# Optimization experiments

Hardware: AMD Instinct MI355X
Metric: run time of the kernel (lower is better)

## Reference

```python
import jax, jax.numpy as jnp
import numpy as np

LATENT = 128   # latent_size
FDIM = 32      # feature_dim per plane
FSIZE = 512    # feature_size -> grid is (FSIZE+1)^2
HID = 256      # hidden_dim
N = 500000     # number of query points
IN_DIM = 3
G = FSIZE + 1
SDF_IN = 3 * FDIM + LATENT + IN_DIM  # 227


def setup_inputs() -> dict:
    key = jax.random.key(0)
    ks = jax.random.split(key, 6)
    x = jax.random.normal(ks[0], (N, LATENT + IN_DIM), jnp.float32)
    # 3 tri-planes, each [FDIM, G, G], init randn*0.01 as in FeaturePlanes
    P = jax.random.normal(ks[1], (3, FDIM, G, G), jnp.float32) * 0.01

    def lin(k, fan_in, fan_out):
        s = 1.0 / np.sqrt(fan_in)
        kw, kb = jax.random.split(k)
        W = jax.random.uniform(kw, (fan_in, fan_out), jnp.float32, -s, s)
        b = jax.random.uniform(kb, (fan_out,), jnp.float32, -s, s)
        return W, b

    W0, b0 = lin(ks[2], SDF_IN, HID)
    W1, b1 = lin(ks[3], HID, HID)
    W2, b2 = lin(ks[4], HID, 1)
    return dict(x=x, P=P, W0=W0, b0=b0, W1=W1, b1=b1, W2=W2, b2=b2)


def _sample_plane(plane, uv):
    """Bilinear grid_sample, align_corners=True, padding_mode='border'.
    plane: [C, G, G]; uv: [Npts, 2] with uv[:,0]->width(x), uv[:,1]->height(y).
    Returns [Npts, C]."""
    g = jnp.clip((uv + 1.0) * 0.5 * (G - 1), 0.0, G - 1)  # unnormalize + border clamp
    gx, gy = g[:, 0], g[:, 1]
    x0f, y0f = jnp.floor(gx), jnp.floor(gy)
    x0 = x0f.astype(jnp.int32)
    y0 = y0f.astype(jnp.int32)
    x1 = jnp.minimum(x0 + 1, G - 1)
    y1 = jnp.minimum(y0 + 1, G - 1)
    wx = gx - x0f
    wy = gy - y0f
    v00 = plane[:, y0, x0]  # [C, Npts]
    v01 = plane[:, y0, x1]
    v10 = plane[:, y1, x0]
    v11 = plane[:, y1, x1]
    top = v00 * (1.0 - wx) + v01 * wx
    bot = v10 * (1.0 - wx) + v11 * wx
    return (top * (1.0 - wy) + bot * wy).T  # [Npts, C]


def reference(x, P, W0, b0, W1, b1, W2, b2):
    in_latents = x[:, :LATENT]
    in_x = x[:, -3:]
    coords = jax.lax.stop_gradient(in_x)  # matches .detach() before grid_sample
    # dimension pairs (0,1), (0,2), (1,2) -> one bilinear lookup each, vmapped
    uv = jnp.stack([coords[:, [0, 1]], coords[:, [0, 2]], coords[:, [1, 2]]])  # [3,N,2]
    feats = jax.vmap(_sample_plane)(P, uv)              # [3, N, FDIM]
    feats = jnp.transpose(feats, (1, 0, 2)).reshape(x.shape[0], 3 * FDIM)
    net_in = jnp.concatenate([in_latents, in_x, feats], axis=-1)  # [N, 227]
    h = jax.nn.relu(net_in @ W0 + b0)
    h = jax.nn.relu(h @ W1 + b1)
    out = (h @ W2 + b2).squeeze(-1)  # [N]
    return out
```

## Files before the change

kernel.cpp:

```cpp
#include <hip/hip_runtime.h>
#include <stdint.h>

#define XDIM 131
#define LATENT 128
#define FDIM 32
#define GSZ 513
#define SDF_IN 227
#define FEAT0 136
#define TROWS 64
#define BSTRIDE 1040

typedef __attribute__((ext_vector_type(8))) short bf16x8;
typedef __attribute__((ext_vector_type(4))) float f32x4;
typedef unsigned int uint32;

__device__ __forceinline__ unsigned short f2bf(float f) {
  uint32 u = __float_as_uint(f);
  u += 0x7fffu + ((u >> 16) & 1u);
  return (unsigned short)(u >> 16);
}
__device__ __forceinline__ float bf2f(unsigned short s) {
  return __uint_as_float(((uint32)s) << 16);
}
__device__ __forceinline__ uint32 pk2bf(float a, float b) {
  return (uint32)f2bf(a) | ((uint32)f2bf(b) << 16);
}

__device__ __forceinline__ int slot16(int r) { return (r * 16) ^ (((r >> 3) & 1) << 5); }
__device__ __forceinline__ int blk_of(int c) { return (c >> 5) * 4 + ((c >> 3) & 3); }
__device__ __forceinline__ int act_byte(int r, int c) {
  return blk_of(c) * BSTRIDE + slot16(r) + (c & 7) * 2;
}

__global__ void prep_pt(const float* __restrict__ P, unsigned short* __restrict__ Pt) {
  int i = blockIdx.x * 256 + threadIdx.x;
  const int CELLS = 3 * GSZ * GSZ;
  if (i >= CELLS) return;
  int pl = i / (GSZ * GSZ);
  int yx = i - pl * (GSZ * GSZ);
  const float* src = P + (size_t)pl * FDIM * GSZ * GSZ + yx;
  const size_t GG = (size_t)GSZ * GSZ;
  uint4* dst = (uint4*)(Pt + (size_t)i * 32);
#pragma unroll
  for (int w = 0; w < 4; ++w) {
    uint4 t;
    t.x = pk2bf(src[(w * 8 + 0) * GG], src[(w * 8 + 1) * GG]);
    t.y = pk2bf(src[(w * 8 + 2) * GG], src[(w * 8 + 3) * GG]);
    t.z = pk2bf(src[(w * 8 + 4) * GG], src[(w * 8 + 5) * GG]);
    t.w = pk2bf(src[(w * 8 + 6) * GG], src[(w * 8 + 7) * GG]);
    dst[w] = t;
  }
}

__global__ void prep_w(const float* __restrict__ W0, const float* __restrict__ W1,
                       unsigned short* __restrict__ W0g, unsigned short* __restrict__ W1g) {
  int i = blockIdx.x * 256 + threadIdx.x;
  int sel = i >> 13;
  int t = i & 8191;
  int kb = t >> 10;
  int g  = (t >> 8) & 3;
  int n  = t & 255;
  float vv[8];
#pragma unroll
  for (int j = 0; j < 8; ++j) {
    int k = kb * 32 + g * 8 + j;
    float val;
    if (sel == 0) {
      int src = (k < 131) ? k : ((k >= FEAT0 && k < FEAT0 + 96) ? k - 5 : -1);
      val = (src >= 0) ? W0[src * 256 + n] : 0.f;
    } else {
      val = W1[k * 256 + n];
    }
    vv[j] = val;
  }
  uint4 o;
  o.x = pk2bf(vv[0], vv[1]);
  o.y = pk2bf(vv[2], vv[3]);
  o.z = pk2bf(vv[4], vv[5]);
  o.w = pk2bf(vv[6], vv[7]);
  unsigned short* dst = (sel == 0 ? W0g : W1g) + (size_t)t * 8;
  *(uint4*)dst = o;
}

__device__ __forceinline__ void gemm_layer(unsigned char* actb,
                                           const unsigned short* __restrict__ Wg,
                                           const float* __restrict__ bias,
                                           int cg, int lr, int lg)
{
  f32x4 acc[4][4];
#pragma unroll
  for (int mf = 0; mf < 4; ++mf)
#pragma unroll
    for (int nf = 0; nf < 4; ++nf) acc[mf][nf] = (f32x4){0.f, 0.f, 0.f, 0.f};

  float bs[4];
#pragma unroll
  for (int nf = 0; nf < 4; ++nf) bs[nf] = bias[cg * 64 + nf * 16 + lr];

#pragma unroll
  for (int kb = 0; kb < 8; ++kb) {
    bf16x8 a[4];
    const int ab = (kb * 4 + lg) * BSTRIDE;
#pragma unroll
    for (int mf = 0; mf < 4; ++mf)
      a[mf] = *(const bf16x8*)(actb + ab + slot16(mf * 16 + lr));
    const unsigned short* wb = Wg + (size_t)(kb * 4 + lg) * 2048 + (size_t)(cg * 64 + lr) * 8;
#pragma unroll
    for (int nf = 0; nf < 4; ++nf) {
      bf16x8 b = *(const bf16x8*)(wb + nf * 128);
#pragma unroll
      for (int mf = 0; mf < 4; ++mf)
        acc[mf][nf] = __builtin_amdgcn_mfma_f32_16x16x32_bf16(a[mf], b, acc[mf][nf], 0, 0, 0);
    }
  }
  __syncthreads();
#pragma unroll
  for (int mf = 0; mf < 4; ++mf)
#pragma unroll
    for (int nf = 0; nf < 4; ++nf) {
      int c = cg * 64 + nf * 16 + lr;
      unsigned char* dst = actb + blk_of(c) * BSTRIDE + (c & 7) * 2;
#pragma unroll
      for (int reg = 0; reg < 4; ++reg) {
        int r = mf * 16 + lg * 4 + reg;
        float vv = fmaxf(acc[mf][nf][reg] + bs[nf], 0.f);
        *(unsigned short*)(dst + slot16(r)) = f2bf(vv);
      }
    }
  __syncthreads();
}

template<int USE_PT>
__global__ __launch_bounds__(256, 4) void sdf_main(
    const float* __restrict__ x, const float* __restrict__ P,
    const unsigned short* __restrict__ Pt,
    const unsigned short* __restrict__ W0g, const unsigned short* __restrict__ W1g,
    const float* __restrict__ b0, const float* __restrict__ b1,
    const float* __restrict__ W2, const float* __restrict__ b2v,
    float* __restrict__ out, int Npts)
{
  __shared__ __align__(16) unsigned char actb[32 * BSTRIDE];

  const int tid = threadIdx.x;
  const int p0 = blockIdx.x * TROWS;

  for (int z = tid; z < 260; z += 256) {
    uint4 zz = {0u, 0u, 0u, 0u};
    if (z < 65) ((uint4*)(actb + 16 * BSTRIDE))[z] = zz;
    else        ((uint4*)(actb + 29 * BSTRIDE))[z - 65] = zz;
  }
  __syncthreads();

#pragma unroll 1
  for (int i = 0; i < 4; ++i) {
    int t = i * 256 + tid;
    int cb = t & 15, r = t >> 4;
    int p = min(p0 + r, Npts - 1);
    const float* src = x + (size_t)p * XDIM + cb * 8;
    uint4 v;
    v.x = pk2bf(src[0], src[1]);
    v.y = pk2bf(src[2], src[3]);
    v.z = pk2bf(src[4], src[5]);
    v.w = pk2bf(src[6], src[7]);
    *(uint4*)(actb + cb * BSTRIDE + slot16(r)) = v;
  }
  if (tid < TROWS) {
    int r = tid;
    int p = min(p0 + r, Npts - 1);
#pragma unroll
    for (int j = 0; j < 3; ++j)
      *(unsigned short*)(actb + act_byte(r, 128 + j)) = f2bf(x[(size_t)p * XDIM + 128 + j]);
  }

  {
    int p_l = tid >> 2;
    int q = tid & 3;
    int p = min(p0 + p_l, Npts - 1);
    const float* xr = x + (size_t)p * XDIM + LATENT;
    float cc0 = xr[0], cc1 = xr[1], cc2 = xr[2];
#pragma unroll
    for (int pl = 0; pl < 3; ++pl) {
      float u = (pl == 2) ? cc1 : cc0;
      float v = (pl == 0) ? cc1 : cc2;
      float gx = fminf(fmaxf((u + 1.f) * 256.f, 0.f), 512.f);
      float gy = fminf(fmaxf((v + 1.f) * 256.f, 0.f), 512.f);
      float x0f = floorf(gx), y0f = floorf(gy);
      int x0 = (int)x0f, y0 = (int)y0f;
      int x1 = min(x0 + 1, GSZ - 1), y1 = min(y0 + 1, GSZ - 1);
      float wx = gx - x0f, wy = gy - y0f;
      float w00 = (1.f - wx) * (1.f - wy), w01 = wx * (1.f - wy);
      float w10 = (1.f - wx) * wy,        w11 = wx * wy;
      const unsigned short* pb = Pt + (size_t)pl * GSZ * GSZ * 32 + q * 8;
      bf16x8 v00 = *(const bf16x8*)(pb + (size_t)(y0 * GSZ + x0) * 32);
      bf16x8 v01 = *(const bf16x8*)(pb + (size_t)(y0 * GSZ + x1) * 32);
      bf16x8 v10 = *(const bf16x8*)(pb + (size_t)(y1 * GSZ + x0) * 32);
      bf16x8 v11 = *(const bf16x8*)(pb + (size_t)(y1 * GSZ + x1) * 32);
      float f[8];
#pragma unroll
      for (int j = 0; j < 8; ++j) {
        f[j] = w00 * bf2f((unsigned short)v00[j])
             + w01 * bf2f((unsigned short)v01[j])
             + w10 * bf2f((unsigned short)v10[j])
             + w11 * bf2f((unsigned short)v11[j]);
      }
      uint4 fv;
      fv.x = pk2bf(f[0], f[1]);
      fv.y = pk2bf(f[2], f[3]);
      fv.z = pk2bf(f[4], f[5]);
      fv.w = pk2bf(f[6], f[7]);
      *(uint4*)(actb + (17 + pl * 4 + q) * BSTRIDE + slot16(p_l)) = fv;
    }
  }
  __syncthreads();

  const int lane = tid & 63, wid = tid >> 6;
  const int lr = lane & 15, lg = lane >> 4;

  gemm_layer(actb, W0g, b0, wid, lr, lg);
  gemm_layer(actb, W1g, b1, wid, lr, lg);

  {
    int p_l = tid >> 2, q = tid & 3;
    float sum = 0.f;
#pragma unroll 2
    for (int m = 0; m < 8; ++m) {
      int cbase = m * 32 + q * 8;
      bf16x8 h = *(const bf16x8*)(actb + (m * 4 + q) * BSTRIDE + slot16(p_l));
      float4 wa = *(const float4*)(W2 + cbase);
      float4 wb = *(const float4*)(W2 + cbase + 4);
      sum += bf2f((unsigned short)h[0]) * wa.x + bf2f((unsigned short)h[1]) * wa.y
           + bf2f((unsigned short)h[2]) * wa.z + bf2f((unsigned short)h[3]) * wa.w
           + bf2f((unsigned short)h[4]) * wb.x + bf2f((unsigned short)h[5]) * wb.y
           + bf2f((unsigned short)h[6]) * wb.z + bf2f((unsigned short)h[7]) * wb.w;
    }
    sum += __shfl_xor(sum, 1);
    sum += __shfl_xor(sum, 2);
    if (q == 0) {
      int p = p0 + p_l;
      if (p < Npts) out[p] = sum + b2v[0];
    }
  }
}

extern "C" void kernel_launch(void* const* d_in, const int* in_sizes, int n_in,
                              void* d_out, int out_size, void* d_ws, size_t ws_size,
                              hipStream_t stream)
{
  const float* x  = (const float*)d_in[0];
  const float* P  = (const float*)d_in[1];
  const float* W0 = (const float*)d_in[2];
  const float* b0 = (const float*)d_in[3];
  const float* W1 = (const float*)d_in[4];
  const float* b1 = (const float*)d_in[5];
  const float* W2 = (const float*)d_in[6];
  const float* b2 = (const float*)d_in[7];
  float* out = (float*)d_out;
  int Npts = in_sizes[0] / XDIM;

  const size_t PT_BYTES = (size_t)3 * GSZ * GSZ * 32 * 2;
  const size_t WG_BYTES = (size_t)8192 * 8 * 2;
  char* ws = (char*)d_ws;
  int use_pt = (ws_size >= PT_BYTES + 2 * WG_BYTES) ? 1 : 0;
  unsigned short *Ptb, *W0g, *W1g;
  if (use_pt) {
    Ptb = (unsigned short*)ws;
    W0g = (unsigned short*)(ws + PT_BYTES);
    W1g = (unsigned short*)(ws + PT_BYTES + WG_BYTES);
  } else {
    Ptb = nullptr;
    W0g = (unsigned short*)ws;
    W1g = (unsigned short*)(ws + WG_BYTES);
  }

  prep_w<<<64, 256, 0, stream>>>(W0, W1, W0g, W1g);
  if (use_pt) prep_pt<<<(3 * GSZ * GSZ + 255) / 256, 256, 0, stream>>>(P, Ptb);

  int nblk = (Npts + TROWS - 1) / TROWS;
  if (use_pt)
    sdf_main<1><<<nblk, 256, 0, stream>>>(x, P, Ptb, W0g, W1g, b0, b1, W2, b2, out, Npts);
  else
    sdf_main<0><<<nblk, 256, 0, stream>>>(x, P, Ptb, W0g, W1g, b0, b1, W2, b2, out, Npts);
}
```

Before: 333.7 us.

## Split tri-plane gather into separate kernel and widen MLP blocks to 512 threads

Adds a standalone gather kernel that computes the bilinear tri-plane features into a bf16 workspace buffer, which the MLP kernel then copies into shared memory. The MLP kernel now runs 512 threads (8 waves), each wave owning 32 output columns instead of 64, to raise latency hiding and occupancy. The aim is to decouple the latency-bound random gathers from the MFMA GEMM phase. It costs an extra global write and read of roughly 96 MB of features plus one more launch, and it depends on the workspace being large enough, with fallback modes kept for smaller workspaces.

Result: no change. 330.0 us (-1.1%).

```diff
diff --git a/kernel.cpp b/kernel.cpp
--- a/kernel.cpp
+++ b/kernel.cpp
@@ -3,14 +3,13 @@
 
 #define XDIM 131
 #define LATENT 128
-#define FDIM 32
 #define GSZ 513
-#define SDF_IN 227
 #define FEAT0 136
 #define TROWS 64
 #define BSTRIDE 1040
 
 typedef __attribute__((ext_vector_type(8))) short bf16x8;
+typedef __attribute__((ext_vector_type(4))) short bf16x4;
 typedef __attribute__((ext_vector_type(4))) float f32x4;
 typedef unsigned int uint32;
 
@@ -28,9 +27,6 @@
 
 __device__ __forceinline__ int slot16(int r) { return (r * 16) ^ (((r >> 3) & 1) << 5); }
 __device__ __forceinline__ int blk_of(int c) { return (c >> 5) * 4 + ((c >> 3) & 3); }
-__device__ __forceinline__ int act_byte(int r, int c) {
-  return blk_of(c) * BSTRIDE + slot16(r) + (c & 7) * 2;
-}
 
 __global__ void prep_pt(const float* __restrict__ P, unsigned short* __restrict__ Pt) {
   int i = blockIdx.x * 256 + threadIdx.x;
@@ -38,7 +34,7 @@
   if (i >= CELLS) return;
   int pl = i / (GSZ * GSZ);
   int yx = i - pl * (GSZ * GSZ);
-  const float* src = P + (size_t)pl * FDIM * GSZ * GSZ + yx;
+  const float* src = P + (size_t)pl * 32 * GSZ * GSZ + yx;
   const size_t GG = (size_t)GSZ * GSZ;
   uint4* dst = (uint4*)(Pt + (size_t)i * 32);
 #pragma unroll
@@ -82,20 +78,75 @@
   *(uint4*)dst = o;
 }
 
+__global__ __launch_bounds__(256) void k_gather(
+    const float* __restrict__ x, const unsigned short* __restrict__ Pt,
+    unsigned short* __restrict__ feats, int Npts)
+{
+  int idx = blockIdx.x * 256 + threadIdx.x;
+  int p = min(idx >> 2, Npts - 1);
+  int q = idx & 3;
+  const float* xr = x + (size_t)p * XDIM + LATENT;
+  float cc0 = xr[0], cc1 = xr[1], cc2 = xr[2];
+
+  const unsigned short* pp[12];
+  float w[12];
+#pragma unroll
+  for (int pl = 0; pl < 3; ++pl) {
+    float u = (pl == 2) ? cc1 : cc0;
+    float v = (pl == 0) ? cc1 : cc2;
+    float gx = fminf(fmaxf((u + 1.f) * 256.f, 0.f), 512.f);
+    float gy = fminf(fmaxf((v + 1.f) * 256.f, 0.f), 512.f);
+    float x0f = floorf(gx), y0f = floorf(gy);
+    int x0 = (int)x0f, y0 = (int)y0f;
+    int x1 = min(x0 + 1, GSZ - 1), y1 = min(y0 + 1, GSZ - 1);
+    float wx = gx - x0f, wy = gy - y0f;
+    w[pl * 4 + 0] = (1.f - wx) * (1.f - wy);
+    w[pl * 4 + 1] = wx * (1.f - wy);
+    w[pl * 4 + 2] = (1.f - wx) * wy;
+    w[pl * 4 + 3] = wx * wy;
+    const unsigned short* pb = Pt + (size_t)pl * GSZ * GSZ * 32 + q * 8;
+    pp[pl * 4 + 0] = pb + (size_t)(y0 * GSZ + x0) * 32;
+    pp[pl * 4 + 1] = pb + (size_t)(y0 * GSZ + x1) * 32;
+    pp[pl * 4 + 2] = pb + (size_t)(y1 * GSZ + x0) * 32;
+    pp[pl * 4 + 3] = pb + (size_t)(y1 * GSZ + x1) * 32;
+  }
+  bf16x8 v[12];
+#pragma unroll
+  for (int j = 0; j < 12; ++j) v[j] = *(const bf16x8*)pp[j];
+
+#pragma unroll
+  for (int pl = 0; pl < 3; ++pl) {
+    float f[8];
+#pragma unroll
+    for (int j = 0; j < 8; ++j) {
+      f[j] = w[pl * 4 + 0] * bf2f((unsigned short)v[pl * 4 + 0][j])
+           + w[pl * 4 + 1] * bf2f((unsigned short)v[pl * 4 + 1][j])
+           + w[pl * 4 + 2] * bf2f((unsigned short)v[pl * 4 + 2][j])
+           + w[pl * 4 + 3] * bf2f((unsigned short)v[pl * 4 + 3][j]);
+    }
+    uint4 fv;
+    fv.x = pk2bf(f[0], f[1]);
+    fv.y = pk2bf(f[2], f[3]);
+    fv.z = pk2bf(f[4], f[5]);
+    fv.w = pk2bf(f[6], f[7]);
+    *(uint4*)(feats + (size_t)p * 96 + pl * 32 + q * 8) = fv;
+  }
+}
+
 __device__ __forceinline__ void gemm_layer(unsigned char* actb,
                                            const unsigned short* __restrict__ Wg,
                                            const float* __restrict__ bias,
                                            int cg, int lr, int lg)
 {
-  f32x4 acc[4][4];
+  f32x4 acc[4][2];
 #pragma unroll
   for (int mf = 0; mf < 4; ++mf)
 #pragma unroll
-    for (int nf = 0; nf < 4; ++nf) acc[mf][nf] = (f32x4){0.f, 0.f, 0.f, 0.f};
-
-  float bs[4];
-#pragma unroll
-  for (int nf = 0; nf < 4; ++nf) bs[nf] = bias[cg * 64 + nf * 16 + lr];
+    for (int nf = 0; nf < 2; ++nf) acc[mf][nf] = (f32x4){0.f, 0.f, 0.f, 0.f};
+
+  float bs[2];
+#pragma unroll
+  for (int nf = 0; nf < 2; ++nf) bs[nf] = bias[cg * 32 + nf * 16 + lr];
 
 #pragma unroll
   for (int kb = 0; kb < 8; ++kb) {
@@ -104,9 +155,9 @@
 #pragma unroll
     for (int mf = 0; mf < 4; ++mf)
       a[mf] = *(const bf16x8*)(actb + ab + slot16(mf * 16 + lr));
-    const unsigned short* wb = Wg + (size_t)(kb * 4 + lg) * 2048 + (size_t)(cg * 64 + lr) * 8;
-#pragma unroll
-    for (int nf = 0; nf < 4; ++nf) {
+    const unsigned short* wb = Wg + (size_t)(kb * 4 + lg) * 2048 + (size_t)(cg * 32 + lr) * 8;
+#pragma unroll
+    for (int nf = 0; nf < 2; ++nf) {
       bf16x8 b = *(const bf16x8*)(wb + nf * 128);
 #pragma unroll
       for (int mf = 0; mf < 4; ++mf)
@@ -117,8 +168,8 @@
 #pragma unroll
   for (int mf = 0; mf < 4; ++mf)
 #pragma unroll
-    for (int nf = 0; nf < 4; ++nf) {
-      int c = cg * 64 + nf * 16 + lr;
+    for (int nf = 0; nf < 2; ++nf) {
+      int c = cg * 32 + nf * 16 + lr;
       unsigned char* dst = actb + blk_of(c) * BSTRIDE + (c & 7) * 2;
 #pragma unroll
       for (int reg = 0; reg < 4; ++reg) {
@@ -130,10 +181,10 @@
   __syncthreads();
 }
 
-template<int USE_PT>
-__global__ __launch_bounds__(256, 4) void sdf_main(
+template<int MODE>
+__global__ __launch_bounds__(512, 4) void sdf_mlp(
     const float* __restrict__ x, const float* __restrict__ P,
-    const unsigned short* __restrict__ Pt,
+    const unsigned short* __restrict__ Pt, const unsigned short* __restrict__ feats,
     const unsigned short* __restrict__ W0g, const unsigned short* __restrict__ W1g,
     const float* __restrict__ b0, const float* __restrict__ b1,
     const float* __restrict__ W2, const float* __restrict__ b2v,
@@ -144,16 +195,16 @@
   const int tid = threadIdx.x;
   const int p0 = blockIdx.x * TROWS;
 
-  for (int z = tid; z < 260; z += 256) {
+  if (tid < 260) {
     uint4 zz = {0u, 0u, 0u, 0u};
-    if (z < 65) ((uint4*)(actb + 16 * BSTRIDE))[z] = zz;
-    else        ((uint4*)(actb + 29 * BSTRIDE))[z - 65] = zz;
+    if (tid < 65) ((uint4*)(actb + 16 * BSTRIDE))[tid] = zz;
+    else          ((uint4*)(actb + 29 * BSTRIDE))[tid - 65] = zz;
   }
   __syncthreads();
 
-#pragma unroll 1
-  for (int i = 0; i < 4; ++i) {
-    int t = i * 256 + tid;
+#pragma unroll
+  for (int i = 0; i < 2; ++i) {
+    int t = i * 512 + tid;
     int cb = t & 15, r = t >> 4;
     int p = min(p0 + r, Npts - 1);
     const float* src = x + (size_t)p * XDIM + cb * 8;
@@ -167,14 +218,24 @@
   if (tid < TROWS) {
     int r = tid;
     int p = min(p0 + r, Npts - 1);
-#pragma unroll
-    for (int j = 0; j < 3; ++j)
-      *(unsigned short*)(actb + act_byte(r, 128 + j)) = f2bf(x[(size_t)p * XDIM + 128 + j]);
-  }
-
-  {
-    int p_l = tid >> 2;
-    int q = tid & 3;
+    const float* xr = x + (size_t)p * XDIM + 128;
+    *(uint32*)(actb + 16 * BSTRIDE + slot16(r)) = pk2bf(xr[0], xr[1]);
+    *(unsigned short*)(actb + 16 * BSTRIDE + slot16(r) + 4) = f2bf(xr[2]);
+  }
+
+  if (MODE == 0) {
+    int r = tid & 63, j0 = tid >> 6;
+    int p = min(p0 + r, Npts - 1);
+#pragma unroll
+    for (int jj = 0; jj < 2; ++jj) {
+      int j = j0 + jj * 8;
+      if (j < 12) {
+        uint4 fv = *(const uint4*)(feats + (size_t)p * 96 + j * 8);
+        *(uint4*)(actb + (17 + j) * BSTRIDE + slot16(r)) = fv;
+      }
+    }
+  } else {
+    int p_l = tid >> 3, q8 = tid & 7;
     int p = min(p0 + p_l, Npts - 1);
     const float* xr = x + (size_t)p * XDIM + LATENT;
     float cc0 = xr[0], cc1 = xr[1], cc2 = xr[2];
@@ -190,52 +251,60 @@
       float wx = gx - x0f, wy = gy - y0f;
       float w00 = (1.f - wx) * (1.f - wy), w01 = wx * (1.f - wy);
       float w10 = (1.f - wx) * wy,        w11 = wx * wy;
-      const unsigned short* pb = Pt + (size_t)pl * GSZ * GSZ * 32 + q * 8;
-      bf16x8 v00 = *(const bf16x8*)(pb + (size_t)(y0 * GSZ + x0) * 32);
-      bf16x8 v01 = *(const bf16x8*)(pb + (size_t)(y0 * GSZ + x1) * 32);
-      bf16x8 v10 = *(const bf16x8*)(pb + (size_t)(y1 * GSZ + x0) * 32);
-      bf16x8 v11 = *(const bf16x8*)(pb + (size_t)(y1 * GSZ + x1) * 32);
-      float f[8];
-#pragma unroll
-      for (int j = 0; j < 8; ++j) {
-        f[j] = w00 * bf2f((unsigned short)v00[j])
-             + w01 * bf2f((unsigned short)v01[j])
-             + w10 * bf2f((unsigned short)v10[j])
-             + w11 * bf2f((unsigned short)v11[j]);
+      float f[4];
+      if (MODE == 1) {
+        const unsigned short* pb = Pt + (size_t)pl * GSZ * GSZ * 32 + q8 * 4;
+        bf16x4 v00 = *(const bf16x4*)(pb + (size_t)(y0 * GSZ + x0) * 32);
+        bf16x4 v01 = *(const bf16x4*)(pb + (size_t)(y0 * GSZ + x1) * 32);
+        bf16x4 v10 = *(const bf16x4*)(pb + (size_t)(y1 * GSZ + x0) * 32);
+        bf16x4 v11 = *(const bf16x4*)(pb + (size_t)(y1 * GSZ + x1) * 32);
+#pragma unroll
+        for (int j = 0; j < 4; ++j) {
+          f[j] = w00 * bf2f((unsigned short)v00[j]) + w01 * bf2f((unsigned short)v01[j])
+               + w10 * bf2f((unsigned short)v10[j]) + w11 * bf2f((unsigned short)v11[j]);
+        }
+      } else {
+#pragma unroll
+        for (int j = 0; j < 4; ++j) {
+          const float* pc = P + (size_t)(pl * 32 + q8 * 4 + j) * GSZ * GSZ;
+          f[j] = w00 * pc[y0 * GSZ + x0] + w01 * pc[y0 * GSZ + x1]
+               + w10 * pc[y1 * GSZ + x0] + w11 * pc[y1 * GSZ + x1];
+        }
       }
-      uint4 fv;
+      int c = FEAT0 + pl * 32 + q8 * 4;
+      uint2 fv;
       fv.x = pk2bf(f[0], f[1]);
       fv.y = pk2bf(f[2], f[3]);
-      fv.z = pk2bf(f[4], f[5]);
-      fv.w = pk2bf(f[6], f[7]);
-      *(uint4*)(actb + (17 + pl * 4 + q) * BSTRIDE + slot16(p_l)) = fv;
+      *(uint2*)(actb + blk_of(c) * BSTRIDE + slot16(p_l) + (c & 7) * 2) = fv;
     }
   }
   __syncthreads();
 
-  const int lane = tid & 63, wid = tid >> 6;
+  const int lane = tid & 63, cg = tid >> 6;
   const int lr = lane & 15, lg = lane >> 4;
 
-  gemm_layer(actb, W0g, b0, wid, lr, lg);
-  gemm_layer(actb, W1g, b1, wid, lr, lg);
+  gemm_layer(actb, W0g, b0, cg, lr, lg);
+  gemm_layer(actb, W1g, b1, cg, lr, lg);
 
   {
-    int p_l = tid >> 2, q = tid & 3;
+    int p_l = tid >> 3, q8 = tid & 7;
     float sum = 0.f;
-#pragma unroll 2
-    for (int m = 0; m < 8; ++m) {
-      int cbase = m * 32 + q * 8;
-      bf16x8 h = *(const bf16x8*)(actb + (m * 4 + q) * BSTRIDE + slot16(p_l));
+#pragma unroll
+    for (int jj = 0; jj < 4; ++jj) {
+      int b = q8 * 4 + jj;
+      int cbase = (b >> 2) * 32 + (b & 3) * 8;
+      bf16x8 h = *(const bf16x8*)(actb + b * BSTRIDE + slot16(p_l));
       float4 wa = *(const float4*)(W2 + cbase);
-      float4 wb = *(const float4*)(W2 + cbase + 4);
+      float4 wb4 = *(const float4*)(W2 + cbase + 4);
       sum += bf2f((unsigned short)h[0]) * wa.x + bf2f((unsigned short)h[1]) * wa.y
            + bf2f((unsigned short)h[2]) * wa.z + bf2f((unsigned short)h[3]) * wa.w
-           + bf2f((unsigned short)h[4]) * wb.x + bf2f((unsigned short)h[5]) * wb.y
-           + bf2f((unsigned short)h[6]) * wb.z + bf2f((unsigned short)h[7]) * wb.w;
+           + bf2f((unsigned short)h[4]) * wb4.x + bf2f((unsigned short)h[5]) * wb4.y
+           + bf2f((unsigned short)h[6]) * wb4.z + bf2f((unsigned short)h[7]) * wb4.w;
     }
     sum += __shfl_xor(sum, 1);
     sum += __shfl_xor(sum, 2);
-    if (q == 0) {
+    sum += __shfl_xor(sum, 4);
+    if (q8 == 0) {
       int p = p0 + p_l;
       if (p < Npts) out[p] = sum + b2v[0];
     }
@@ -259,25 +328,37 @@
 
   const size_t PT_BYTES = (size_t)3 * GSZ * GSZ * 32 * 2;
   const size_t WG_BYTES = (size_t)8192 * 8 * 2;
+  const size_t FT_BYTES = (size_t)Npts * 96 * 2;
   char* ws = (char*)d_ws;
-  int use_pt = (ws_size >= PT_BYTES + 2 * WG_BYTES) ? 1 : 0;
-  unsigned short *Ptb, *W0g, *W1g;
-  if (use_pt) {
+
+  int mode;
+  unsigned short *Ptb = nullptr, *W0g, *W1g, *ft = nullptr;
+  if (ws_size >= PT_BYTES + 2 * WG_BYTES + FT_BYTES) {
+    mode = 0;
+    Ptb = (unsigned short*)ws;
+    W0g = (unsigned short*)(ws + PT_BYTES);
+    W1g = (unsigned short*)(ws + PT_BYTES + WG_BYTES);
+    ft  = (unsigned short*)(ws + PT_BYTES + 2 * WG_BYTES);
+  } else if (ws_size >= PT_BYTES + 2 * WG_BYTES) {
+    mode = 1;
     Ptb = (unsigned short*)ws;
     W0g = (unsigned short*)(ws + PT_BYTES);
     W1g = (unsigned short*)(ws + PT_BYTES + WG_BYTES);
   } else {
-    Ptb = nullptr;
+    mode = 2;
     W0g = (unsigned short*)ws;
     W1g = (unsigned short*)(ws + WG_BYTES);
   }
 
   prep_w<<<64, 256, 0, stream>>>(W0, W1, W0g, W1g);
-  if (use_pt) prep_pt<<<(3 * GSZ * GSZ + 255) / 256, 256, 0, stream>>>(P, Ptb);
+  if (mode != 2) prep_pt<<<(3 * GSZ * GSZ + 255) / 256, 256, 0, stream>>>(P, Ptb);
+  if (mode == 0) k_gather<<<(Npts * 4 + 255) / 256, 256, 0, stream>>>(x, Ptb, ft, Npts);
 
   int nblk = (Npts + TROWS - 1) / TROWS;
-  if (use_pt)
-    sdf_main<1><<<nblk, 256, 0, stream>>>(x, P, Ptb, W0g, W1g, b0, b1, W2, b2, out, Npts);
+  if (mode == 0)
+    sdf_mlp<0><<<nblk, 512, 0, stream>>>(x, P, Ptb, ft, W0g, W1g, b0, b1, W2, b2, out, Npts);
+  else if (mode == 1)
+    sdf_mlp<1><<<nblk, 512, 0, stream>>>(x, P, Ptb, ft, W0g, W1g, b0, b1, W2, b2, out, Npts);
   else
-    sdf_main<0><<<nblk, 256, 0, stream>>>(x, P, Ptb, W0g, W1g, b0, b1, W2, b2, out, Npts);
-}
+    sdf_mlp<2><<<nblk, 512, 0, stream>>>(x, P, Ptb, ft, W0g, W1g, b0, b1, W2, b2, out, Npts);
+}
```

## Make SDF kernel persistent with register prefetch of next tile

Applied to the files above, without the earlier changes.

Converts the one-tile-per-block kernel into a persistent kernel with 512 blocks of 512 threads that loop over 64-point tiles. While the current tile runs its two MFMA layers, the x rows and bf16 plane corner values for the next tile are loaded into registers, to hide global and gather latency behind compute. Each wave now computes 32 output columns instead of 64. The extra prefetch registers may lower occupancy, and with a single LDS buffer each tile needs extra barriers.

Measured after the change: 799.4 us. 2.4x slower.

```diff
diff --git a/kernel.cpp b/kernel.cpp
--- a/kernel.cpp
+++ b/kernel.cpp
@@ -3,14 +3,14 @@
 
 #define XDIM 131
 #define LATENT 128
-#define FDIM 32
 #define GSZ 513
-#define SDF_IN 227
 #define FEAT0 136
 #define TROWS 64
 #define BSTRIDE 1040
+#define NBLK 512
 
 typedef __attribute__((ext_vector_type(8))) short bf16x8;
+typedef __attribute__((ext_vector_type(4))) short bf16x4;
 typedef __attribute__((ext_vector_type(4))) float f32x4;
 typedef unsigned int uint32;
 
@@ -28,9 +28,6 @@
 
 __device__ __forceinline__ int slot16(int r) { return (r * 16) ^ (((r >> 3) & 1) << 5); }
 __device__ __forceinline__ int blk_of(int c) { return (c >> 5) * 4 + ((c >> 3) & 3); }
-__device__ __forceinline__ int act_byte(int r, int c) {
-  return blk_of(c) * BSTRIDE + slot16(r) + (c & 7) * 2;
-}
 
 __global__ void prep_pt(const float* __restrict__ P, unsigned short* __restrict__ Pt) {
   int i = blockIdx.x * 256 + threadIdx.x;
@@ -38,7 +35,7 @@
   if (i >= CELLS) return;
   int pl = i / (GSZ * GSZ);
   int yx = i - pl * (GSZ * GSZ);
-  const float* src = P + (size_t)pl * FDIM * GSZ * GSZ + yx;
+  const float* src = P + (size_t)pl * 32 * GSZ * GSZ + yx;
   const size_t GG = (size_t)GSZ * GSZ;
   uint4* dst = (uint4*)(Pt + (size_t)i * 32);
 #pragma unroll
@@ -87,15 +84,11 @@
                                            const float* __restrict__ bias,
                                            int cg, int lr, int lg)
 {
-  f32x4 acc[4][4];
+  f32x4 acc[4][2];
 #pragma unroll
   for (int mf = 0; mf < 4; ++mf)
 #pragma unroll
-    for (int nf = 0; nf < 4; ++nf) acc[mf][nf] = (f32x4){0.f, 0.f, 0.f, 0.f};
-
-  float bs[4];
-#pragma unroll
-  for (int nf = 0; nf < 4; ++nf) bs[nf] = bias[cg * 64 + nf * 16 + lr];
+    for (int nf = 0; nf < 2; ++nf) acc[mf][nf] = (f32x4){0.f, 0.f, 0.f, 0.f};
 
 #pragma unroll
   for (int kb = 0; kb < 8; ++kb) {
@@ -104,21 +97,24 @@
 #pragma unroll
     for (int mf = 0; mf < 4; ++mf)
       a[mf] = *(const bf16x8*)(actb + ab + slot16(mf * 16 + lr));
-    const unsigned short* wb = Wg + (size_t)(kb * 4 + lg) * 2048 + (size_t)(cg * 64 + lr) * 8;
-#pragma unroll
-    for (int nf = 0; nf < 4; ++nf) {
+    const unsigned short* wb = Wg + (size_t)(kb * 4 + lg) * 2048 + (size_t)(cg * 32 + lr) * 8;
+#pragma unroll
+    for (int nf = 0; nf < 2; ++nf) {
       bf16x8 b = *(const bf16x8*)(wb + nf * 128);
 #pragma unroll
       for (int mf = 0; mf < 4; ++mf)
         acc[mf][nf] = __builtin_amdgcn_mfma_f32_16x16x32_bf16(a[mf], b, acc[mf][nf], 0, 0, 0);
     }
   }
+  float bs[2];
+#pragma unroll
+  for (int nf = 0; nf < 2; ++nf) bs[nf] = bias[cg * 32 + nf * 16 + lr];
   __syncthreads();
 #pragma unroll
   for (int mf = 0; mf < 4; ++mf)
 #pragma unroll
-    for (int nf = 0; nf < 4; ++nf) {
-      int c = cg * 64 + nf * 16 + lr;
+    for (int nf = 0; nf < 2; ++nf) {
+      int c = cg * 32 + nf * 16 + lr;
       unsigned char* dst = actb + blk_of(c) * BSTRIDE + (c & 7) * 2;
 #pragma unroll
       for (int reg = 0; reg < 4; ++reg) {
@@ -131,113 +127,154 @@
 }
 
 template<int USE_PT>
-__global__ __launch_bounds__(256, 4) void sdf_main(
+__global__ __launch_bounds__(512, 4) void sdf_fused(
     const float* __restrict__ x, const float* __restrict__ P,
     const unsigned short* __restrict__ Pt,
     const unsigned short* __restrict__ W0g, const unsigned short* __restrict__ W1g,
     const float* __restrict__ b0, const float* __restrict__ b1,
     const float* __restrict__ W2, const float* __restrict__ b2v,
-    float* __restrict__ out, int Npts)
+    float* __restrict__ out, int Npts, int ntiles)
 {
   __shared__ __align__(16) unsigned char actb[32 * BSTRIDE];
 
   const int tid = threadIdx.x;
-  const int p0 = blockIdx.x * TROWS;
-
-  for (int z = tid; z < 260; z += 256) {
-    uint4 zz = {0u, 0u, 0u, 0u};
-    if (z < 65) ((uint4*)(actb + 16 * BSTRIDE))[z] = zz;
-    else        ((uint4*)(actb + 29 * BSTRIDE))[z - 65] = zz;
-  }
-  __syncthreads();
-
-#pragma unroll 1
-  for (int i = 0; i < 4; ++i) {
-    int t = i * 256 + tid;
-    int cb = t & 15, r = t >> 4;
-    int p = min(p0 + r, Npts - 1);
-    const float* src = x + (size_t)p * XDIM + cb * 8;
-    uint4 v;
-    v.x = pk2bf(src[0], src[1]);
-    v.y = pk2bf(src[2], src[3]);
-    v.z = pk2bf(src[4], src[5]);
-    v.w = pk2bf(src[6], src[7]);
-    *(uint4*)(actb + cb * BSTRIDE + slot16(r)) = v;
-  }
-  if (tid < TROWS) {
-    int r = tid;
-    int p = min(p0 + r, Npts - 1);
-#pragma unroll
-    for (int j = 0; j < 3; ++j)
-      *(unsigned short*)(actb + act_byte(r, 128 + j)) = f2bf(x[(size_t)p * XDIM + 128 + j]);
-  }
-
-  {
-    int p_l = tid >> 2;
-    int q = tid & 3;
-    int p = min(p0 + p_l, Npts - 1);
+  const int G = gridDim.x;
+  const int lane = tid & 63, cg = tid >> 6;
+  const int lr = lane & 15, lg = lane >> 4;
+  const int p_l8 = tid >> 3, q8 = tid & 7;
+
+  float xs[16];
+  float c0 = 0.f, c1 = 0.f, c2 = 0.f;
+  float wxv[3], wyv[3];
+  bf16x4 gv[12];
+
+  auto ISSUE = [&](int t) {
+    int pbase = t * TROWS;
+#pragma unroll
+    for (int k = 0; k < 2; ++k) {
+      int tt = k * 512 + tid;
+      int cb = tt & 15, r = tt >> 4;
+      int p = min(pbase + r, Npts - 1);
+      const float* src = x + (size_t)p * XDIM + cb * 8;
+#pragma unroll
+      for (int j = 0; j < 8; ++j) xs[k * 8 + j] = src[j];
+    }
+    int p = min(pbase + p_l8, Npts - 1);
     const float* xr = x + (size_t)p * XDIM + LATENT;
-    float cc0 = xr[0], cc1 = xr[1], cc2 = xr[2];
+    c0 = xr[0]; c1 = xr[1]; c2 = xr[2];
 #pragma unroll
     for (int pl = 0; pl < 3; ++pl) {
-      float u = (pl == 2) ? cc1 : cc0;
-      float v = (pl == 0) ? cc1 : cc2;
+      float u = (pl == 2) ? c1 : c0;
+      float v = (pl == 0) ? c1 : c2;
       float gx = fminf(fmaxf((u + 1.f) * 256.f, 0.f), 512.f);
       float gy = fminf(fmaxf((v + 1.f) * 256.f, 0.f), 512.f);
       float x0f = floorf(gx), y0f = floorf(gy);
       int x0 = (int)x0f, y0 = (int)y0f;
       int x1 = min(x0 + 1, GSZ - 1), y1 = min(y0 + 1, GSZ - 1);
-      float wx = gx - x0f, wy = gy - y0f;
+      wxv[pl] = gx - x0f; wyv[pl] = gy - y0f;
+      if (USE_PT) {
+        const unsigned short* pb = Pt + (size_t)pl * GSZ * GSZ * 32 + q8 * 4;
+        gv[pl * 4 + 0] = *(const bf16x4*)(pb + (size_t)(y0 * GSZ + x0) * 32);
+        gv[pl * 4 + 1] = *(const bf16x4*)(pb + (size_t)(y0 * GSZ + x1) * 32);
+        gv[pl * 4 + 2] = *(const bf16x4*)(pb + (size_t)(y1 * GSZ + x0) * 32);
+        gv[pl * 4 + 3] = *(const bf16x4*)(pb + (size_t)(y1 * GSZ + x1) * 32);
+      } else {
+#pragma unroll
+        for (int j = 0; j < 4; ++j) {
+          const float* pc = P + (size_t)(pl * 32 + q8 * 4 + j) * GSZ * GSZ;
+          float w00 = (1.f - wxv[pl]) * (1.f - wyv[pl]), w01 = wxv[pl] * (1.f - wyv[pl]);
+          float w10 = (1.f - wxv[pl]) * wyv[pl],         w11 = wxv[pl] * wyv[pl];
+          float f = w00 * pc[y0 * GSZ + x0] + w01 * pc[y0 * GSZ + x1]
+                  + w10 * pc[y1 * GSZ + x0] + w11 * pc[y1 * GSZ + x1];
+          short s = (short)f2bf(f);
+          bf16x4 tmp = gv[pl * 4 + j & 3];  (void)tmp;
+          gv[pl * 4 + 0][j] = s;
+        }
+        gv[pl * 4 + 1] = (bf16x4){0,0,0,0};
+        gv[pl * 4 + 2] = (bf16x4){0,0,0,0};
+        gv[pl * 4 + 3] = (bf16x4){0,0,0,0};
+        wxv[pl] = 0.f; wyv[pl] = 0.f;
+      }
+    }
+  };
+
+  auto STAGE_WRITE = [&]() {
+    if (tid < 195) {
+      uint4 zz = {0u, 0u, 0u, 0u};
+      ((uint4*)(actb + 29 * BSTRIDE))[tid] = zz;
+    }
+#pragma unroll
+    for (int k = 0; k < 2; ++k) {
+      int tt = k * 512 + tid;
+      int cb = tt & 15, r = tt >> 4;
+      uint4 v;
+      v.x = pk2bf(xs[k * 8 + 0], xs[k * 8 + 1]);
+      v.y = pk2bf(xs[k * 8 + 2], xs[k * 8 + 3]);
+      v.z = pk2bf(xs[k * 8 + 4], xs[k * 8 + 5]);
+      v.w = pk2bf(xs[k * 8 + 6], xs[k * 8 + 7]);
+      *(uint4*)(actb + cb * BSTRIDE + slot16(r)) = v;
+    }
+    if (q8 == 0) {
+      uint4 v;
+      v.x = pk2bf(c0, c1);
+      v.y = pk2bf(c2, 0.f);
+      v.z = 0u; v.w = 0u;
+      *(uint4*)(actb + 16 * BSTRIDE + slot16(p_l8)) = v;
+    }
+#pragma unroll
+    for (int pl = 0; pl < 3; ++pl) {
+      float wx = wxv[pl], wy = wyv[pl];
       float w00 = (1.f - wx) * (1.f - wy), w01 = wx * (1.f - wy);
       float w10 = (1.f - wx) * wy,        w11 = wx * wy;
-      const unsigned short* pb = Pt + (size_t)pl * GSZ * GSZ * 32 + q * 8;
-      bf16x8 v00 = *(const bf16x8*)(pb + (size_t)(y0 * GSZ + x0) * 32);
-      bf16x8 v01 = *(const bf16x8*)(pb + (size_t)(y0 * GSZ + x1) * 32);
-      bf16x8 v10 = *(const bf16x8*)(pb + (size_t)(y1 * GSZ + x0) * 32);
-      bf16x8 v11 = *(const bf16x8*)(pb + (size_t)(y1 * GSZ + x1) * 32);
-      float f[8];
-#pragma unroll
-      for (int j = 0; j < 8; ++j) {
-        f[j] = w00 * bf2f((unsigned short)v00[j])
-             + w01 * bf2f((unsigned short)v01[j])
-             + w10 * bf2f((unsigned short)v10[j])
-             + w11 * bf2f((unsigned short)v11[j]);
-      }
-      uint4 fv;
+      float f[4];
+#pragma unroll
+      for (int j = 0; j < 4; ++j) {
+        f[j] = w00 * bf2f((unsigned short)gv[pl * 4 + 0][j])
+             + w01 * bf2f((unsigned short)gv[pl * 4 + 1][j])
+             + w10 * bf2f((unsigned short)gv[pl * 4 + 2][j])
+             + w11 * bf2f((unsigned short)gv[pl * 4 + 3][j]);
+      }
+      int c = FEAT0 + pl * 32 + q8 * 4;
+      uint2 fv;
       fv.x = pk2bf(f[0], f[1]);
       fv.y = pk2bf(f[2], f[3]);
-      fv.z = pk2bf(f[4], f[5]);
-      fv.w = pk2bf(f[6], f[7]);
-      *(uint4*)(actb + (17 + pl * 4 + q) * BSTRIDE + slot16(p_l)) = fv;
-    }
-  }
-  __syncthreads();
-
-  const int lane = tid & 63, wid = tid >> 6;
-  const int lr = lane & 15, lg = lane >> 4;
-
-  gemm_layer(actb, W0g, b0, wid, lr, lg);
-  gemm_layer(actb, W1g, b1, wid, lr, lg);
-
-  {
-    int p_l = tid >> 2, q = tid & 3;
-    float sum = 0.f;
-#pragma unroll 2
-    for (int m = 0; m < 8; ++m) {
-      int cbase = m * 32 + q * 8;
-      bf16x8 h = *(const bf16x8*)(actb + (m * 4 + q) * BSTRIDE + slot16(p_l));
-      float4 wa = *(const float4*)(W2 + cbase);
-      float4 wb = *(const float4*)(W2 + cbase + 4);
-      sum += bf2f((unsigned short)h[0]) * wa.x + bf2f((unsigned short)h[1]) * wa.y
-           + bf2f((unsigned short)h[2]) * wa.z + bf2f((unsigned short)h[3]) * wa.w
-           + bf2f((unsigned short)h[4]) * wb.x + bf2f((unsigned short)h[5]) * wb.y
-           + bf2f((unsigned short)h[6]) * wb.z + bf2f((unsigned short)h[7]) * wb.w;
-    }
-    sum += __shfl_xor(sum, 1);
-    sum += __shfl_xor(sum, 2);
-    if (q == 0) {
-      int p = p0 + p_l;
-      if (p < Npts) out[p] = sum + b2v[0];
+      *(uint2*)(actb + blk_of(c) * BSTRIDE + slot16(p_l8) + (c & 7) * 2) = fv;
+    }
+  };
+
+  int tile = blockIdx.x;
+  if (tile < ntiles) ISSUE(tile);
+
+  for (; tile < ntiles; tile += G) {
+    __syncthreads();
+    STAGE_WRITE();
+    if (tile + G < ntiles) ISSUE(tile + G);
+    __syncthreads();
+
+    gemm_layer(actb, W0g, b0, cg, lr, lg);
+    gemm_layer(actb, W1g, b1, cg, lr, lg);
+
+    {
+      float sum = 0.f;
+#pragma unroll
+      for (int jj = 0; jj < 4; ++jj) {
+        int b = q8 * 4 + jj;
+        int cbase = (b >> 2) * 32 + (b & 3) * 8;
+        bf16x8 h = *(const bf16x8*)(actb + b * BSTRIDE + slot16(p_l8));
+        float4 wa = *(const float4*)(W2 + cbase);
+        float4 wb4 = *(const float4*)(W2 + cbase + 4);
+        sum += bf2f((unsigned short)h[0]) * wa.x + bf2f((unsigned short)h[1]) * wa.y
+             + bf2f((unsigned short)h[2]) * wa.z + bf2f((unsigned short)h[3]) * wa.w
+             + bf2f((unsigned short)h[4]) * wb4.x + bf2f((unsigned short)h[5]) * wb4.y
+             + bf2f((unsigned short)h[6]) * wb4.z + bf2f((unsigned short)h[7]) * wb4.w;
+      }
+      sum += __shfl_xor(sum, 1);
+      sum += __shfl_xor(sum, 2);
+      sum += __shfl_xor(sum, 4);
+      if (q8 == 0) {
+        int p = tile * TROWS + p_l8;
+        if (p < Npts) out[p] = sum + b2v[0];
+      }
     }
   }
 }
@@ -256,18 +293,19 @@
   const float* b2 = (const float*)d_in[7];
   float* out = (float*)d_out;
   int Npts = in_sizes[0] / XDIM;
+  int ntiles = (Npts + TROWS - 1) / TROWS;
 
   const size_t PT_BYTES = (size_t)3 * GSZ * GSZ * 32 * 2;
   const size_t WG_BYTES = (size_t)8192 * 8 * 2;
   char* ws = (char*)d_ws;
+
   int use_pt = (ws_size >= PT_BYTES + 2 * WG_BYTES) ? 1 : 0;
-  unsigned short *Ptb, *W0g, *W1g;
+  unsigned short *Ptb = nullptr, *W0g, *W1g;
   if (use_pt) {
     Ptb = (unsigned short*)ws;
     W0g = (unsigned short*)(ws + PT_BYTES);
     W1g = (unsigned short*)(ws + PT_BYTES + WG_BYTES);
   } else {
-    Ptb = nullptr;
     W0g = (unsigned short*)ws;
     W1g = (unsigned short*)(ws + WG_BYTES);
   }
@@ -275,9 +313,9 @@
   prep_w<<<64, 256, 0, stream>>>(W0, W1, W0g, W1g);
   if (use_pt) prep_pt<<<(3 * GSZ * GSZ + 255) / 256, 256, 0, stream>>>(P, Ptb);
 
-  int nblk = (Npts + TROWS - 1) / TROWS;
+  int nblk = ntiles < NBLK ? ntiles : NBLK;
   if (use_pt)
-    sdf_main<1><<<nblk, 256, 0, stream>>>(x, P, Ptb, W0g, W1g, b0, b1, W2, b2, out, Npts);
+    sdf_fused<1><<<nblk, 512, 0, stream>>>(x, P, Ptb, W0g, W1g, b0, b1, W2, b2, out, Npts, ntiles);
   else
-    sdf_main<0><<<nblk, 256, 0, stream>>>(x, P, Ptb, W0g, W1g, b0, b1, W2, b2, out, Npts);
-}
+    sdf_fused<0><<<nblk, 512, 0, stream>>>(x, P, Ptb, W0g, W1g, b0, b1, W2, b2, out, Npts, ntiles);
+}
```

## Restructure MLP tile to 128 threads, fuse final layer into second GEMM epilogue

Applied to the files above, without the earlier changes.

Rewrites the main kernel to use 128-thread blocks, each wave covering two 64-column groups. Layer-1 output goes to a separate LDS region, which removes the in-place read/write syncs. The W2 dot product is folded into the layer-2 epilogue with shuffle reductions, so layer-2 activations are never written back. It also adds a real fallback path that samples fp32 P directly. The trade-off is larger LDS per block (64KB) and fewer threads, which may lower occupancy and latency hiding for the gather phase.

After: 408.9 us. 1.23x slower.

```diff
diff --git a/kernel.cpp b/kernel.cpp
--- a/kernel.cpp
+++ b/kernel.cpp
@@ -2,13 +2,11 @@
 #include <stdint.h>
 
 #define XDIM 131
-#define LATENT 128
-#define FDIM 32
 #define GSZ 513
-#define SDF_IN 227
-#define FEAT0 136
 #define TROWS 64
-#define BSTRIDE 1040
+#define H_OFF   30720
+#define SC_OFF  63488
+#define LDS_BYTES 64000
 
 typedef __attribute__((ext_vector_type(8))) short bf16x8;
 typedef __attribute__((ext_vector_type(4))) float f32x4;
@@ -25,12 +23,7 @@
 __device__ __forceinline__ uint32 pk2bf(float a, float b) {
   return (uint32)f2bf(a) | ((uint32)f2bf(b) << 16);
 }
-
 __device__ __forceinline__ int slot16(int r) { return (r * 16) ^ (((r >> 3) & 1) << 5); }
-__device__ __forceinline__ int blk_of(int c) { return (c >> 5) * 4 + ((c >> 3) & 3); }
-__device__ __forceinline__ int act_byte(int r, int c) {
-  return blk_of(c) * BSTRIDE + slot16(r) + (c & 7) * 2;
-}
 
 __global__ void prep_pt(const float* __restrict__ P, unsigned short* __restrict__ Pt) {
   int i = blockIdx.x * 256 + threadIdx.x;
@@ -38,7 +31,7 @@
   if (i >= CELLS) return;
   int pl = i / (GSZ * GSZ);
   int yx = i - pl * (GSZ * GSZ);
-  const float* src = P + (size_t)pl * FDIM * GSZ * GSZ + yx;
+  const float* src = P + (size_t)pl * 32 * GSZ * GSZ + yx;
   const size_t GG = (size_t)GSZ * GSZ;
   uint4* dst = (uint4*)(Pt + (size_t)i * 32);
 #pragma unroll
@@ -66,7 +59,7 @@
     int k = kb * 32 + g * 8 + j;
     float val;
     if (sel == 0) {
-      int src = (k < 131) ? k : ((k >= FEAT0 && k < FEAT0 + 96) ? k - 5 : -1);
+      int src = (k < 131) ? k : ((k >= 136 && k < 232) ? k - 5 : -1);
       val = (src >= 0) ? W0[src * 256 + n] : 0.f;
     } else {
       val = W1[k * 256 + n];
@@ -82,56 +75,8 @@
   *(uint4*)dst = o;
 }
 
-__device__ __forceinline__ void gemm_layer(unsigned char* actb,
-                                           const unsigned short* __restrict__ Wg,
-                                           const float* __restrict__ bias,
-                                           int cg, int lr, int lg)
-{
-  f32x4 acc[4][4];
-#pragma unroll
-  for (int mf = 0; mf < 4; ++mf)
-#pragma unroll
-    for (int nf = 0; nf < 4; ++nf) acc[mf][nf] = (f32x4){0.f, 0.f, 0.f, 0.f};
-
-  float bs[4];
-#pragma unroll
-  for (int nf = 0; nf < 4; ++nf) bs[nf] = bias[cg * 64 + nf * 16 + lr];
-
-#pragma unroll
-  for (int kb = 0; kb < 8; ++kb) {
-    bf16x8 a[4];
-    const int ab = (kb * 4 + lg) * BSTRIDE;
-#pragma unroll
-    for (int mf = 0; mf < 4; ++mf)
-      a[mf] = *(const bf16x8*)(actb + ab + slot16(mf * 16 + lr));
-    const unsigned short* wb = Wg + (size_t)(kb * 4 + lg) * 2048 + (size_t)(cg * 64 + lr) * 8;
-#pragma unroll
-    for (int nf = 0; nf < 4; ++nf) {
-      bf16x8 b = *(const bf16x8*)(wb + nf * 128);
-#pragma unroll
-      for (int mf = 0; mf < 4; ++mf)
-        acc[mf][nf] = __builtin_amdgcn_mfma_f32_16x16x32_bf16(a[mf], b, acc[mf][nf], 0, 0, 0);
-    }
-  }
-  __syncthreads();
-#pragma unroll
-  for (int mf = 0; mf < 4; ++mf)
-#pragma unroll
-    for (int nf = 0; nf < 4; ++nf) {
-      int c = cg * 64 + nf * 16 + lr;
-      unsigned char* dst = actb + blk_of(c) * BSTRIDE + (c & 7) * 2;
-#pragma unroll
-      for (int reg = 0; reg < 4; ++reg) {
-        int r = mf * 16 + lg * 4 + reg;
-        float vv = fmaxf(acc[mf][nf][reg] + bs[nf], 0.f);
-        *(unsigned short*)(dst + slot16(r)) = f2bf(vv);
-      }
-    }
-  __syncthreads();
-}
-
 template<int USE_PT>
-__global__ __launch_bounds__(256, 4) void sdf_main(
+__global__ __launch_bounds__(128) void sdf_tile(
     const float* __restrict__ x, const float* __restrict__ P,
     const unsigned short* __restrict__ Pt,
     const unsigned short* __restrict__ W0g, const unsigned short* __restrict__ W1g,
@@ -139,22 +84,17 @@
     const float* __restrict__ W2, const float* __restrict__ b2v,
     float* __restrict__ out, int Npts)
 {
-  __shared__ __align__(16) unsigned char actb[32 * BSTRIDE];
+  __shared__ __align__(16) unsigned char lds[LDS_BYTES];
 
   const int tid = threadIdx.x;
   const int p0 = blockIdx.x * TROWS;
-
-  for (int z = tid; z < 260; z += 256) {
-    uint4 zz = {0u, 0u, 0u, 0u};
-    if (z < 65) ((uint4*)(actb + 16 * BSTRIDE))[z] = zz;
-    else        ((uint4*)(actb + 29 * BSTRIDE))[z - 65] = zz;
-  }
-  __syncthreads();
-
-#pragma unroll 1
-  for (int i = 0; i < 4; ++i) {
-    int t = i * 256 + tid;
-    int cb = t & 15, r = t >> 4;
+  const int lane = tid & 63, wv = tid >> 6;
+  const int lr = lane & 15, lg = lane >> 4;
+
+#pragma unroll
+  for (int i = 0; i < 8; ++i) {
+    int t = i * 128 + tid;
+    int r = t & 63, cb = t >> 6;
     int p = min(p0 + r, Npts - 1);
     const float* src = x + (size_t)p * XDIM + cb * 8;
     uint4 v;
@@ -162,21 +102,27 @@
     v.y = pk2bf(src[2], src[3]);
     v.z = pk2bf(src[4], src[5]);
     v.w = pk2bf(src[6], src[7]);
-    *(uint4*)(actb + cb * BSTRIDE + slot16(r)) = v;
-  }
-  if (tid < TROWS) {
-    int r = tid;
-    int p = min(p0 + r, Npts - 1);
-#pragma unroll
-    for (int j = 0; j < 3; ++j)
-      *(unsigned short*)(actb + act_byte(r, 128 + j)) = f2bf(x[(size_t)p * XDIM + 128 + j]);
-  }
-
-  {
-    int p_l = tid >> 2;
+    *(uint4*)(lds + cb * 1024 + slot16(r)) = v;
+  }
+  if (tid < 64) {
+    int p = min(p0 + tid, Npts - 1);
+    const float* xr = x + (size_t)p * XDIM + 128;
+    uint4 v;
+    v.x = pk2bf(xr[0], xr[1]);
+    v.y = pk2bf(xr[2], 0.f);
+    v.z = 0u; v.w = 0u;
+    *(uint4*)(lds + 16 * 1024 + slot16(tid)) = v;
+  } else {
+    uint4 z = {0u, 0u, 0u, 0u};
+    ((uint4*)(lds + 29 * 1024))[tid - 64] = z;
+  }
+
+#pragma unroll
+  for (int g = 0; g < 2; ++g) {
+    int pt = g * 32 + (tid >> 2);
     int q = tid & 3;
-    int p = min(p0 + p_l, Npts - 1);
-    const float* xr = x + (size_t)p * XDIM + LATENT;
+    int p = min(p0 + pt, Npts - 1);
+    const float* xr = x + (size_t)p * XDIM + 128;
     float cc0 = xr[0], cc1 = xr[1], cc2 = xr[2];
 #pragma unroll
     for (int pl = 0; pl < 3; ++pl) {
@@ -190,55 +136,144 @@
       float wx = gx - x0f, wy = gy - y0f;
       float w00 = (1.f - wx) * (1.f - wy), w01 = wx * (1.f - wy);
       float w10 = (1.f - wx) * wy,        w11 = wx * wy;
-      const unsigned short* pb = Pt + (size_t)pl * GSZ * GSZ * 32 + q * 8;
-      bf16x8 v00 = *(const bf16x8*)(pb + (size_t)(y0 * GSZ + x0) * 32);
-      bf16x8 v01 = *(const bf16x8*)(pb + (size_t)(y0 * GSZ + x1) * 32);
-      bf16x8 v10 = *(const bf16x8*)(pb + (size_t)(y1 * GSZ + x0) * 32);
-      bf16x8 v11 = *(const bf16x8*)(pb + (size_t)(y1 * GSZ + x1) * 32);
       float f[8];
-#pragma unroll
-      for (int j = 0; j < 8; ++j) {
-        f[j] = w00 * bf2f((unsigned short)v00[j])
-             + w01 * bf2f((unsigned short)v01[j])
-             + w10 * bf2f((unsigned short)v10[j])
-             + w11 * bf2f((unsigned short)v11[j]);
+      if (USE_PT) {
+        const unsigned short* pb = Pt + (size_t)pl * GSZ * GSZ * 32 + q * 8;
+        bf16x8 v00 = *(const bf16x8*)(pb + (size_t)(y0 * GSZ + x0) * 32);
+        bf16x8 v01 = *(const bf16x8*)(pb + (size_t)(y0 * GSZ + x1) * 32);
+        bf16x8 v10 = *(const bf16x8*)(pb + (size_t)(y1 * GSZ + x0) * 32);
+        bf16x8 v11 = *(const bf16x8*)(pb + (size_t)(y1 * GSZ + x1) * 32);
+#pragma unroll
+        for (int j = 0; j < 8; ++j) {
+          f[j] = w00 * bf2f((unsigned short)v00[j]) + w01 * bf2f((unsigned short)v01[j])
+               + w10 * bf2f((unsigned short)v10[j]) + w11 * bf2f((unsigned short)v11[j]);
+        }
+      } else {
+#pragma unroll
+        for (int j = 0; j < 8; ++j) {
+          const float* pc = P + (size_t)(pl * 32 + q * 8 + j) * GSZ * GSZ;
+          f[j] = w00 * pc[y0 * GSZ + x0] + w01 * pc[y0 * GSZ + x1]
+               + w10 * pc[y1 * GSZ + x0] + w11 * pc[y1 * GSZ + x1];
+        }
       }
       uint4 fv;
       fv.x = pk2bf(f[0], f[1]);
       fv.y = pk2bf(f[2], f[3]);
       fv.z = pk2bf(f[4], f[5]);
       fv.w = pk2bf(f[6], f[7]);
-      *(uint4*)(actb + (17 + pl * 4 + q) * BSTRIDE + slot16(p_l)) = fv;
+      *(uint4*)(lds + (17 + pl * 4 + q) * 1024 + slot16(pt)) = fv;
     }
   }
   __syncthreads();
 
-  const int lane = tid & 63, wid = tid >> 6;
-  const int lr = lane & 15, lg = lane >> 4;
-
-  gemm_layer(actb, W0g, b0, wid, lr, lg);
-  gemm_layer(actb, W1g, b1, wid, lr, lg);
-
-  {
-    int p_l = tid >> 2, q = tid & 3;
-    float sum = 0.f;
-#pragma unroll 2
-    for (int m = 0; m < 8; ++m) {
-      int cbase = m * 32 + q * 8;
-      bf16x8 h = *(const bf16x8*)(actb + (m * 4 + q) * BSTRIDE + slot16(p_l));
-      float4 wa = *(const float4*)(W2 + cbase);
-      float4 wb = *(const float4*)(W2 + cbase + 4);
-      sum += bf2f((unsigned short)h[0]) * wa.x + bf2f((unsigned short)h[1]) * wa.y
-           + bf2f((unsigned short)h[2]) * wa.z + bf2f((unsigned short)h[3]) * wa.w
-           + bf2f((unsigned short)h[4]) * wb.x + bf2f((unsigned short)h[5]) * wb.y
-           + bf2f((unsigned short)h[6]) * wb.z + bf2f((unsigned short)h[7]) * wb.w;
-    }
-    sum += __shfl_xor(sum, 1);
-    sum += __shfl_xor(sum, 2);
-    if (q == 0) {
-      int p = p0 + p_l;
-      if (p < Npts) out[p] = sum + b2v[0];
-    }
+#pragma unroll
+  for (int gi = 0; gi < 2; ++gi) {
+    const int cg = wv * 2 + gi;
+    f32x4 acc[4][4];
+#pragma unroll
+    for (int mf = 0; mf < 4; ++mf)
+#pragma unroll
+      for (int nf = 0; nf < 4; ++nf) acc[mf][nf] = (f32x4){0.f, 0.f, 0.f, 0.f};
+#pragma unroll
+    for (int kb = 0; kb < 8; ++kb) {
+      bf16x8 a[4];
+      int ib = kb * 4 + lg;
+      if (ib > 28) ib = 29;
+#pragma unroll
+      for (int mf = 0; mf < 4; ++mf)
+        a[mf] = *(const bf16x8*)(lds + ib * 1024 + slot16(mf * 16 + lr));
+      const unsigned short* wb = W0g + ((size_t)(kb * 4 + lg) * 256 + cg * 64 + lr) * 8;
+#pragma unroll
+      for (int nf = 0; nf < 4; ++nf) {
+        bf16x8 b = *(const bf16x8*)(wb + nf * 128);
+#pragma unroll
+        for (int mf = 0; mf < 4; ++mf)
+          acc[mf][nf] = __builtin_amdgcn_mfma_f32_16x16x32_bf16(a[mf], b, acc[mf][nf], 0, 0, 0);
+      }
+    }
+#pragma unroll
+    for (int nf = 0; nf < 4; ++nf) {
+      int col = cg * 64 + nf * 16 + lr;
+      float bs = b0[col];
+      unsigned char* base = lds + H_OFF + (col >> 3) * 1024 + (col & 7) * 2;
+#pragma unroll
+      for (int mf = 0; mf < 4; ++mf)
+#pragma unroll
+        for (int reg = 0; reg < 4; ++reg) {
+          int row = mf * 16 + lg * 4 + reg;
+          *(unsigned short*)(base + slot16(row)) = f2bf(fmaxf(acc[mf][nf][reg] + bs, 0.f));
+        }
+    }
+  }
+  __syncthreads();
+
+  float part[4][4];
+#pragma unroll
+  for (int mf = 0; mf < 4; ++mf)
+#pragma unroll
+    for (int reg = 0; reg < 4; ++reg) part[mf][reg] = 0.f;
+
+#pragma unroll
+  for (int gi = 0; gi < 2; ++gi) {
+    const int cg = wv * 2 + gi;
+    f32x4 acc[4][4];
+#pragma unroll
+    for (int mf = 0; mf < 4; ++mf)
+#pragma unroll
+      for (int nf = 0; nf < 4; ++nf) acc[mf][nf] = (f32x4){0.f, 0.f, 0.f, 0.f};
+#pragma unroll
+    for (int kb = 0; kb < 8; ++kb) {
+      bf16x8 a[4];
+#pragma unroll
+      for (int mf = 0; mf < 4; ++mf)
+        a[mf] = *(const bf16x8*)(lds + H_OFF + (kb * 4 + lg) * 1024 + slot16(mf * 16 + lr));
+      const unsigned short* wb = W1g + ((size_t)(kb * 4 + lg) * 256 + cg * 64 + lr) * 8;
+#pragma unroll
+      for (int nf = 0; nf < 4; ++nf) {
+        bf16x8 b = *(const bf16x8*)(wb + nf * 128);
+#pragma unroll
+        for (int mf = 0; mf < 4; ++mf)
+          acc[mf][nf] = __builtin_amdgcn_mfma_f32_16x16x32_bf16(a[mf], b, acc[mf][nf], 0, 0, 0);
+      }
+    }
+#pragma unroll
+    for (int nf = 0; nf < 4; ++nf) {
+      int col = cg * 64 + nf * 16 + lr;
+      float bs = b1[col];
+      float w2v = W2[col];
+#pragma unroll
+      for (int mf = 0; mf < 4; ++mf)
+#pragma unroll
+        for (int reg = 0; reg < 4; ++reg)
+          part[mf][reg] += fmaxf(acc[mf][nf][reg] + bs, 0.f) * w2v;
+    }
+  }
+#pragma unroll
+  for (int mf = 0; mf < 4; ++mf)
+#pragma unroll
+    for (int reg = 0; reg < 4; ++reg) {
+      float v = part[mf][reg];
+      v += __shfl_xor(v, 1);
+      v += __shfl_xor(v, 2);
+      v += __shfl_xor(v, 4);
+      v += __shfl_xor(v, 8);
+      part[mf][reg] = v;
+    }
+  if (lr == 0) {
+    float* sc = (float*)(lds + SC_OFF) + wv * 64;
+#pragma unroll
+    for (int mf = 0; mf < 4; ++mf) {
+      float4 pv;
+      pv.x = part[mf][0]; pv.y = part[mf][1]; pv.z = part[mf][2]; pv.w = part[mf][3];
+      *(float4*)(sc + mf * 16 + lg * 4) = pv;
+    }
+  }
+  __syncthreads();
+  if (tid < 64) {
+    const float* sc = (const float*)(lds + SC_OFF);
+    float s = sc[tid] + sc[64 + tid] + b2v[0];
+    int p = p0 + tid;
+    if (p < Npts) out[p] = s;
   }
 }
 
@@ -260,14 +295,14 @@
   const size_t PT_BYTES = (size_t)3 * GSZ * GSZ * 32 * 2;
   const size_t WG_BYTES = (size_t)8192 * 8 * 2;
   char* ws = (char*)d_ws;
+
   int use_pt = (ws_size >= PT_BYTES + 2 * WG_BYTES) ? 1 : 0;
-  unsigned short *Ptb, *W0g, *W1g;
+  unsigned short *Ptb = nullptr, *W0g, *W1g;
   if (use_pt) {
     Ptb = (unsigned short*)ws;
     W0g = (unsigned short*)(ws + PT_BYTES);
     W1g = (unsigned short*)(ws + PT_BYTES + WG_BYTES);
   } else {
-    Ptb = nullptr;
     W0g = (unsigned short*)ws;
     W1g = (unsigned short*)(ws + WG_BYTES);
   }
@@ -277,7 +312,7 @@
 
   int nblk = (Npts + TROWS - 1) / TROWS;
   if (use_pt)
-    sdf_main<1><<<nblk, 256, 0, stream>>>(x, P, Ptb, W0g, W1g, b0, b1, W2, b2, out, Npts);
+    sdf_tile<1><<<nblk, 128, 0, stream>>>(x, P, Ptb, W0g, W1g, b0, b1, W2, b2, out, Npts);
   else
-    sdf_main<0><<<nblk, 256, 0, stream>>>(x, P, Ptb, W0g, W1g, b0, b1, W2, b2, out, Npts);
-}
+    sdf_tile<0><<<nblk, 128, 0, stream>>>(x, P, Ptb, W0g, W1g, b0, b1, W2, b2, out, Npts);
+}
```
